# Kernel optimization log

Hardware: AMD Instinct MI355X
Metric: run time of the kernel (lower is better)

## Reference

```python
import jax, jax.numpy as jnp
import numpy as np

B, N, NC = 16, 102000, 35        # batch, raw YOLOv7@1280 predictions, num classes
IMG = 1280                        # input image size
CONF_THRESH = 0.25
IOU_THRESH = 0.45
PRE_TOPK = 1024                   # candidates kept before IoU suppression (yolov7 max_nms analogue)
MAX_DET = 300                     # padded detections per image (yolov7 max_det)


def setup_inputs() -> dict:
    key = jax.random.key(0)
    kxy, kwh, kobj, kcls = jax.random.split(key, 4)
    xy = jax.random.uniform(kxy, (B, N, 2), dtype=jnp.float32) * IMG        # box centers in pixels
    wh = jax.random.uniform(kwh, (B, N, 2), dtype=jnp.float32) * 96.0 + 4.0  # box sizes
    obj = jax.random.uniform(kobj, (B, N, 1), dtype=jnp.float32)            # objectness
    cls = jax.random.uniform(kcls, (B, N, NC), dtype=jnp.float32)           # class scores
    pred = jnp.concatenate([xy, wh, obj, cls], axis=-1)  # [B, N, 5+NC]
    return {"pred": pred}


def _xywh2xyxy(xywh):
    xy, wh = xywh[..., :2], xywh[..., 2:4]
    return jnp.concatenate([xy - wh * 0.5, xy + wh * 0.5], axis=-1)


def _iou_matrix(b):
    # b: [K, 4] xyxy -> [K, K] pairwise IoU
    area = jnp.clip(b[:, 2] - b[:, 0], 0.0) * jnp.clip(b[:, 3] - b[:, 1], 0.0)
    lt = jnp.maximum(b[:, None, :2], b[None, :, :2])
    rb = jnp.minimum(b[:, None, 2:], b[None, :, 2:])
    wh = jnp.clip(rb - lt, 0.0)
    inter = wh[..., 0] * wh[..., 1]
    return inter / (area[:, None] + area[None, :] - inter + 1e-7)


def _nms_single(boxes, scores, cls_id):
    # boxes: [N,4] xyxy, scores: [N] (0 where below conf thresh), cls_id: [N] float
    s, idx = jax.lax.top_k(scores, PRE_TOPK)
    b = boxes[idx]
    c = cls_id[idx]
    iou = _iou_matrix(b)              # [K, K]
    valid = s > 0.0
    ar = jnp.arange(PRE_TOPK)

    def body(suppressed, i):
        keep_i = valid[i] & ~suppressed[i]
        suppressed = suppressed | (keep_i & (iou[i] > IOU_THRESH) & (ar > i))
        return suppressed, keep_i

    _, keep = jax.lax.scan(body, jnp.zeros(PRE_TOPK, bool), ar)
    final = jnp.where(keep, s, 0.0)
    fs, fidx = jax.lax.top_k(final, MAX_DET)
    # [MAX_DET, 6] = x1, y1, x2, y2, conf, cls (conf==0 rows are padding)
    return jnp.concatenate([b[fidx], fs[:, None], c[fidx][:, None]], axis=-1)


def reference(pred):
    # yolov7 non_max_suppression, class-agnostic, best-class per box
    boxes = _xywh2xyxy(pred[..., :4])                    # [B, N, 4]
    obj = pred[..., 4]                                   # [B, N]
    cls_scores = pred[..., 5:] * obj[..., None]          # obj_conf * cls_conf
    conf = jnp.max(cls_scores, axis=-1)                  # [B, N]
    cls_id = jnp.argmax(cls_scores, axis=-1).astype(pred.dtype)
    cand = (obj > CONF_THRESH) & (conf > CONF_THRESH)    # candidate filter
    scores = jnp.where(cand, conf, 0.0)
    return jax.vmap(_nms_single)(boxes, scores, cls_id)  # [B, MAX_DET, 6]
```

## Files before the change

kernel.cpp:

```cpp
#include <hip/hip_runtime.h>
#include <stdint.h>

#define BB 16
#define NN 102000
#define NCLS 35
#define RSTRIDE 40
#define PRE 1024
#define CAP 2048
#define MAXDET 300
#define NBUCK 4096
#define CONF_T 0.25f
#define IOU_T 0.45f
#define BUCK_BASE 0x3E800000u
#define SROWS 256

#define SCORES_OFF ((size_t)0)
#define SCORES_BYTES ((size_t)BB * NN * 4)
#define GHIST_OFF (SCORES_OFF + SCORES_BYTES)
#define GHIST_BYTES ((size_t)BB * NBUCK * 4)
#define CUT_OFF (GHIST_OFF + GHIST_BYTES)
#define BOXES_OFF (CUT_OFF + 64)
#define BOXES_BYTES ((size_t)BB * PRE * 16)
#define SVAL_OFF (BOXES_OFF + BOXES_BYTES)
#define SVAL_BYTES ((size_t)BB * PRE * 4)
#define CLS_OFF (SVAL_OFF + SVAL_BYTES)
#define CLS_BYTES ((size_t)BB * PRE * 4)
#define MASK_OFF (CLS_OFF + CLS_BYTES)
#define MASK_BYTES ((size_t)BB * PRE * 16 * 8)

__global__ __launch_bounds__(256) void k_score(const float* __restrict__ pred,
                                               float* __restrict__ scores,
                                               unsigned int* __restrict__ ghist) {
    __shared__ float4 lds4[SROWS * 9];
    int b = blockIdx.y, tid = threadIdx.x;
    int rowBase = blockIdx.x * SROWS;
    int nrows = NN - rowBase; if (nrows > SROWS) nrows = SROWS;
    const float4* gp = (const float4*)(pred + ((size_t)b * NN + rowBase) * RSTRIDE);
    int nf4 = nrows * 9;
    for (int it = tid; it < nf4; it += 256) {
        int r = it / 9;
        int c = it - r * 9;
        lds4[r * 9 + c] = gp[r * 10 + 1 + c];
    }
    __syncthreads();
    if (tid < nrows) {
        const float4* row4 = &lds4[tid * 9];
        float4 v0 = row4[0];
        float obj = v0.x;
        float score = 0.0f;
        if (obj > CONF_T) {
            float best = v0.y * obj;
            best = fmaxf(best, v0.z * obj);
            best = fmaxf(best, v0.w * obj);
#pragma unroll
            for (int c = 1; c < 9; ++c) {
                float4 v = row4[c];
                best = fmaxf(best, v.x * obj);
                best = fmaxf(best, v.y * obj);
                best = fmaxf(best, v.z * obj);
                best = fmaxf(best, v.w * obj);
            }
            if (best > CONF_T) score = best;
        }
        scores[(size_t)b * NN + rowBase + tid] = score;
        if (score > 0.0f) {
            unsigned int bits = __float_as_uint(score);
            unsigned int bk = (bits - BUCK_BASE) >> 12;
            if (bk > NBUCK - 1u) bk = NBUCK - 1u;
            atomicAdd(&ghist[b * NBUCK + bk], 1u);
        }
    }
}

__global__ __launch_bounds__(1024) void k_cut(const unsigned int* __restrict__ ghist,
                                              unsigned int* __restrict__ cutv) {
    __shared__ int sA[1024], sB[1024];
    __shared__ int cutB;
    int b = blockIdx.x, tid = threadIdx.x;
    if (tid == 0) cutB = 0;
    __syncthreads();
    const unsigned int* gh = ghist + b * NBUCK;
    int h0 = gh[4 * tid + 0], h1 = gh[4 * tid + 1];
    int h2 = gh[4 * tid + 2], h3 = gh[4 * tid + 3];
    sA[tid] = h0 + h1 + h2 + h3;
    __syncthreads();
    int* src = sA;
    int* dst = sB;
    for (int off = 1; off < 1024; off <<= 1) {
        int x = src[tid];
        if (tid + off < 1024) x += src[tid + off];
        dst[tid] = x;
        __syncthreads();
        int* t_ = src; src = dst; dst = t_;
    }
    int nxt = (tid + 1 < 1024) ? src[tid + 1] : 0;
    int s3 = h3 + nxt;
    int s2 = h2 + s3;
    int s1 = h1 + s2;
    int s0 = h0 + s1;
    if (s0 >= PRE && s1 < PRE) cutB = 4 * tid + 0;
    if (s1 >= PRE && s2 < PRE) cutB = 4 * tid + 1;
    if (s2 >= PRE && s3 < PRE) cutB = 4 * tid + 2;
    if (s3 >= PRE && nxt < PRE) cutB = 4 * tid + 3;
    __syncthreads();
    if (tid == 0) cutv[b] = (unsigned int)cutB;
}

__global__ __launch_bounds__(1024) void k_sort(const float* __restrict__ scores,
                                               const unsigned int* __restrict__ cutv,
                                               const float* __restrict__ pred,
                                               float4* __restrict__ boxesWS,
                                               float* __restrict__ svalWS,
                                               float* __restrict__ clsWS) {
    __shared__ unsigned long long keys[CAP];
    __shared__ unsigned int nloc;
    int b = blockIdx.x, tid = threadIdx.x;
    unsigned int cut = cutv[b];
    if (tid == 0) nloc = 0u;
    for (int k = tid; k < CAP; k += 1024) keys[k] = 0ull;
    __syncthreads();
    const float4* sb4 = (const float4*)(scores + (size_t)b * NN);
    for (int it = tid; it < NN / 4; it += 1024) {
        float4 s4 = sb4[it];
        float sv[4] = {s4.x, s4.y, s4.z, s4.w};
#pragma unroll
        for (int u = 0; u < 4; ++u) {
            float s = sv[u];
            if (s > 0.0f) {
                unsigned int bits = __float_as_uint(s);
                unsigned int bk = (bits - BUCK_BASE) >> 12;
                if (bk > NBUCK - 1u) bk = NBUCK - 1u;
                if (bk >= cut) {
                    unsigned int pos = atomicAdd(&nloc, 1u);
                    unsigned int idx = (unsigned int)(it * 4 + u);
                    if (pos < CAP)
                        keys[pos] = ((unsigned long long)bits << 32) |
                                    (unsigned int)(~idx);
                }
            }
        }
    }
    __syncthreads();
    for (int k = 2; k <= CAP; k <<= 1) {
        for (int j = k >> 1; j > 0; j >>= 1) {
            int p = ((tid & ~(j - 1)) << 1) | (tid & (j - 1));
            int q = p | j;
            unsigned long long a = keys[p], c = keys[q];
            bool desc = (p & k) == 0;
            bool sw = desc ? (a < c) : (a > c);
            if (sw) { keys[p] = c; keys[q] = a; }
            __syncthreads();
        }
    }
    unsigned long long key = keys[tid];
    unsigned int bits = (unsigned int)(key >> 32);
    unsigned int idx = ~(unsigned int)key;
    float sc = __uint_as_float(bits);
    if (bits == 0u || idx >= NN) { idx = 0; sc = 0.0f; }
    const float4* row = (const float4*)(pred + ((size_t)b * NN + idx) * RSTRIDE);
    float4 r0 = row[0];
    float4 r1 = row[1];
    float obj = r1.x;
    float best = r1.y * obj; int bj = 0;
    float p1 = r1.z * obj; if (p1 > best) { best = p1; bj = 1; }
    float p2 = r1.w * obj; if (p2 > best) { best = p2; bj = 2; }
#pragma unroll
    for (int kk = 2; kk <= 9; ++kk) {
        float4 r = row[kk];
        int base = (kk - 2) * 4 + 3;
        float q0 = r.x * obj; if (q0 > best) { best = q0; bj = base + 0; }
        float q1 = r.y * obj; if (q1 > best) { best = q1; bj = base + 1; }
        float q2 = r.z * obj; if (q2 > best) { best = q2; bj = base + 2; }
        float q3 = r.w * obj; if (q3 > best) { best = q3; bj = base + 3; }
    }
    float hx = r0.z * 0.5f;
    float hy = r0.w * 0.5f;
    boxesWS[b * PRE + tid] = make_float4(r0.x - hx, r0.y - hy, r0.x + hx, r0.y + hy);
    svalWS[b * PRE + tid] = sc;
    clsWS[b * PRE + tid] = (float)bj;
}

__global__ __launch_bounds__(256) void k_mask(const float4* __restrict__ boxesWS,
                                              const float* __restrict__ svalWS,
                                              unsigned long long* __restrict__ maskC) {
    __shared__ float bx1[PRE], by1[PRE], bx2[PRE], by2[PRE], bar[PRE], bsv[PRE];
    int b = blockIdx.y, tid = threadIdx.x;
    for (int i = tid; i < PRE; i += 256) {
        float4 bx = boxesWS[b * PRE + i];
        bx1[i] = bx.x; by1[i] = bx.y; bx2[i] = bx.z; by2[i] = bx.w;
        float aw = fmaxf(bx.z - bx.x, 0.0f);
        float ah = fmaxf(bx.w - bx.y, 0.0f);
        bar[i] = aw * ah;
        bsv[i] = svalWS[b * PRE + i];
    }
    __syncthreads();
    int j = blockIdx.x * 4 + (tid >> 6);
    int lane = tid & 63;
    float jx1 = bx1[j], jy1 = by1[j], jx2 = bx2[j], jy2 = by2[j], ja = bar[j];
    unsigned long long* out = maskC + ((size_t)b * PRE + j) * 16;
    for (int c = 0; c < 16; ++c) {
        unsigned long long word = 0ull;
        if (c * 64 < j) {
            int i = c * 64 + lane;
            bool bit = false;
            if (i < j && bsv[i] > 0.0f) {
                float ltx = fmaxf(bx1[i], jx1), lty = fmaxf(by1[i], jy1);
                float rbx = fminf(bx2[i], jx2), rby = fminf(by2[i], jy2);
                float wx = fmaxf(rbx - ltx, 0.0f);
                float wy = fmaxf(rby - lty, 0.0f);
                float inter = wx * wy;
                float denom = ((bar[i] + ja) - inter) + 1e-7f;
                bit = (inter / denom) > IOU_T;
            }
            word = __ballot(bit);
        }
        if (lane == 0) out[c] = word;
    }
}

__global__ __launch_bounds__(1024) void k_nms_out(const float4* __restrict__ boxesWS,
                                                  const float* __restrict__ svalWS,
                                                  const float* __restrict__ clsWS,
                                                  const unsigned long long* __restrict__ maskC,
                                                  float* __restrict__ out) {
    __shared__ unsigned long long supp[16], nsupp[16];
    __shared__ int changed;
    __shared__ int wtot[16], woff[17];
    int b = blockIdx.x, tid = threadIdx.x;
    int lane = tid & 63, w = tid >> 6;
    unsigned long long cm[16];
    const unsigned long long* mrow = maskC + ((size_t)b * PRE + tid) * 16;
#pragma unroll
    for (int k = 0; k < 16; ++k) cm[k] = mrow[k];
    float sv = svalWS[b * PRE + tid];
    if (tid < 16) supp[tid] = 0ull;
    __syncthreads();
    for (int it = 0; it < PRE + 2; ++it) {
        bool nb = false;
#pragma unroll
        for (int k = 0; k < 16; ++k) nb |= ((cm[k] & ~supp[k]) != 0ull);
        unsigned long long word = __ballot(nb);
        __syncthreads();
        if (lane == 0) nsupp[w] = word;
        if (tid == 0) changed = 0;
        __syncthreads();
        if (tid < 16) {
            if (nsupp[tid] != supp[tid]) changed = 1;
            supp[tid] = nsupp[tid];
        }
        __syncthreads();
        if (!changed) break;
    }
    bool keep = (sv > 0.0f) && !((supp[w] >> lane) & 1ull);
    unsigned long long km = __ballot(keep);
    int lp = __popcll(km & ((lane == 0) ? 0ull : ((1ull << lane) - 1ull)));
    if (lane == 0) wtot[w] = __popcll(km);
    __syncthreads();
    if (tid == 0) {
        int acc = 0;
        for (int k = 0; k < 16; ++k) { woff[k] = acc; acc += wtot[k]; }
        woff[16] = acc;
    }
    __syncthreads();
    int K = woff[16];
    int keptExcl = woff[w] + lp;
    int slot = keep ? keptExcl : (K + (tid - keptExcl));
    if (slot < MAXDET) {
        float4 bx = boxesWS[b * PRE + tid];
        float cv = clsWS[b * PRE + tid];
        float* o = out + ((size_t)b * MAXDET + slot) * 6;
        o[0] = bx.x; o[1] = bx.y; o[2] = bx.z; o[3] = bx.w;
        o[4] = keep ? sv : 0.0f;
        o[5] = cv;
    }
}

extern "C" void kernel_launch(void* const* d_in, const int* in_sizes, int n_in,
                              void* d_out, int out_size, void* d_ws, size_t ws_size,
                              hipStream_t stream) {
    const float* pred = (const float*)d_in[0];
    float* out = (float*)d_out;
    char* ws = (char*)d_ws;
    float* scores = (float*)(ws + SCORES_OFF);
    unsigned int* ghist = (unsigned int*)(ws + GHIST_OFF);
    unsigned int* cutv = (unsigned int*)(ws + CUT_OFF);
    float4* boxesWS = (float4*)(ws + BOXES_OFF);
    float* svalWS = (float*)(ws + SVAL_OFF);
    float* clsWS = (float*)(ws + CLS_OFF);
    unsigned long long* maskC = (unsigned long long*)(ws + MASK_OFF);

    hipMemsetAsync(ws + GHIST_OFF, 0, GHIST_BYTES, stream);
    k_score<<<dim3((NN + SROWS - 1) / SROWS, BB), 256, 0, stream>>>(pred, scores, ghist);
    k_cut<<<BB, 1024, 0, stream>>>(ghist, cutv);
    k_sort<<<BB, 1024, 0, stream>>>(scores, cutv, pred, boxesWS, svalWS, clsWS);
    k_mask<<<dim3(PRE / 4, BB), 256, 0, stream>>>(boxesWS, svalWS, maskC);
    k_nms_out<<<BB, 1024, 0, stream>>>(boxesWS, svalWS, clsWS, maskC, out);
}
```

Measured before the change: 434.7 us.

## Use per-wave tiles in score kernel and fuse cut with sort kernel

The score kernel now gives each 64-lane wave its own 64-row tile. The wave copies full 40-float rows contiguously into LDS with no block-wide barrier, in place of the strided 9-of-10 float4 gather. The separate histogram-cut kernel is merged into the sort kernel, so the cut bucket stays in shared memory, which removes one launch and the global cut round-trip. The trade-off is that the score kernel now also loads the unused first float4 of each row, and the fused kernel uses more shared memory.

```diff
diff --git a/kernel.cpp b/kernel.cpp
--- a/kernel.cpp
+++ b/kernel.cpp
@@ -12,14 +12,13 @@
 #define CONF_T 0.25f
 #define IOU_T 0.45f
 #define BUCK_BASE 0x3E800000u
-#define SROWS 256
+#define TROWS 64
 
 #define SCORES_OFF ((size_t)0)
 #define SCORES_BYTES ((size_t)BB * NN * 4)
 #define GHIST_OFF (SCORES_OFF + SCORES_BYTES)
 #define GHIST_BYTES ((size_t)BB * NBUCK * 4)
-#define CUT_OFF (GHIST_OFF + GHIST_BYTES)
-#define BOXES_OFF (CUT_OFF + 64)
+#define BOXES_OFF (GHIST_OFF + GHIST_BYTES)
 #define BOXES_BYTES ((size_t)BB * PRE * 16)
 #define SVAL_OFF (BOXES_OFF + BOXES_BYTES)
 #define SVAL_BYTES ((size_t)BB * PRE * 4)
@@ -31,21 +30,24 @@
 __global__ __launch_bounds__(256) void k_score(const float* __restrict__ pred,
                                                float* __restrict__ scores,
                                                unsigned int* __restrict__ ghist) {
-    __shared__ float4 lds4[SROWS * 9];
-    int b = blockIdx.y, tid = threadIdx.x;
-    int rowBase = blockIdx.x * SROWS;
-    int nrows = NN - rowBase; if (nrows > SROWS) nrows = SROWS;
+    __shared__ float4 lds4[4 * TROWS * 10];
+    int b = blockIdx.y;
+    int wv = threadIdx.x >> 6, lane = threadIdx.x & 63;
+    int tile = blockIdx.x * 4 + wv;
+    int rowBase = tile * TROWS;
+    if (rowBase >= NN) return;
+    int nrows = NN - rowBase; if (nrows > TROWS) nrows = TROWS;
+    int nf4 = nrows * 10;
     const float4* gp = (const float4*)(pred + ((size_t)b * NN + rowBase) * RSTRIDE);
-    int nf4 = nrows * 9;
-    for (int it = tid; it < nf4; it += 256) {
-        int r = it / 9;
-        int c = it - r * 9;
-        lds4[r * 9 + c] = gp[r * 10 + 1 + c];
-    }
-    __syncthreads();
-    if (tid < nrows) {
-        const float4* row4 = &lds4[tid * 9];
-        float4 v0 = row4[0];
+    float4* wlds = &lds4[wv * TROWS * 10];
+#pragma unroll
+    for (int k = 0; k < 10; ++k) {
+        int idx = k * 64 + lane;
+        if (idx < nf4) wlds[idx] = gp[idx];
+    }
+    if (lane < nrows) {
+        const float4* row4 = &wlds[lane * 10];
+        float4 v0 = row4[1];
         float obj = v0.x;
         float score = 0.0f;
         if (obj > CONF_T) {
@@ -53,7 +55,7 @@
             best = fmaxf(best, v0.z * obj);
             best = fmaxf(best, v0.w * obj);
 #pragma unroll
-            for (int c = 1; c < 9; ++c) {
+            for (int c = 2; c < 10; ++c) {
                 float4 v = row4[c];
                 best = fmaxf(best, v.x * obj);
                 best = fmaxf(best, v.y * obj);
@@ -62,7 +64,7 @@
             }
             if (best > CONF_T) score = best;
         }
-        scores[(size_t)b * NN + rowBase + tid] = score;
+        scores[(size_t)b * NN + rowBase + lane] = score;
         if (score > 0.0f) {
             unsigned int bits = __float_as_uint(score);
             unsigned int bk = (bits - BUCK_BASE) >> 12;
@@ -72,12 +74,19 @@
     }
 }
 
-__global__ __launch_bounds__(1024) void k_cut(const unsigned int* __restrict__ ghist,
-                                              unsigned int* __restrict__ cutv) {
+__global__ __launch_bounds__(1024) void k_cutsort(const unsigned int* __restrict__ ghist,
+                                                  const float* __restrict__ scores,
+                                                  const float* __restrict__ pred,
+                                                  float4* __restrict__ boxesWS,
+                                                  float* __restrict__ svalWS,
+                                                  float* __restrict__ clsWS) {
+    __shared__ unsigned long long keys[CAP];
     __shared__ int sA[1024], sB[1024];
     __shared__ int cutB;
+    __shared__ unsigned int nloc;
     int b = blockIdx.x, tid = threadIdx.x;
-    if (tid == 0) cutB = 0;
+    if (tid == 0) { cutB = 0; nloc = 0u; }
+    keys[tid] = 0ull; keys[tid + 1024] = 0ull;
     __syncthreads();
     const unsigned int* gh = ghist + b * NBUCK;
     int h0 = gh[4 * tid + 0], h1 = gh[4 * tid + 1];
@@ -103,22 +112,7 @@
     if (s2 >= PRE && s3 < PRE) cutB = 4 * tid + 2;
     if (s3 >= PRE && nxt < PRE) cutB = 4 * tid + 3;
     __syncthreads();
-    if (tid == 0) cutv[b] = (unsigned int)cutB;
-}
-
-__global__ __launch_bounds__(1024) void k_sort(const float* __restrict__ scores,
-                                               const unsigned int* __restrict__ cutv,
-                                               const float* __restrict__ pred,
-                                               float4* __restrict__ boxesWS,
-                                               float* __restrict__ svalWS,
-                                               float* __restrict__ clsWS) {
-    __shared__ unsigned long long keys[CAP];
-    __shared__ unsigned int nloc;
-    int b = blockIdx.x, tid = threadIdx.x;
-    unsigned int cut = cutv[b];
-    if (tid == 0) nloc = 0u;
-    for (int k = tid; k < CAP; k += 1024) keys[k] = 0ull;
-    __syncthreads();
+    unsigned int cut = (unsigned int)cutB;
     const float4* sb4 = (const float4*)(scores + (size_t)b * NN);
     for (int it = tid; it < NN / 4; it += 1024) {
         float4 s4 = sb4[it];
@@ -283,16 +277,16 @@
     char* ws = (char*)d_ws;
     float* scores = (float*)(ws + SCORES_OFF);
     unsigned int* ghist = (unsigned int*)(ws + GHIST_OFF);
-    unsigned int* cutv = (unsigned int*)(ws + CUT_OFF);
     float4* boxesWS = (float4*)(ws + BOXES_OFF);
     float* svalWS = (float*)(ws + SVAL_OFF);
     float* clsWS = (float*)(ws + CLS_OFF);
     unsigned long long* maskC = (unsigned long long*)(ws + MASK_OFF);
 
+    int tilesPerBatch = (NN + TROWS - 1) / TROWS;
+    int blocksX = (tilesPerBatch + 3) / 4;
     hipMemsetAsync(ws + GHIST_OFF, 0, GHIST_BYTES, stream);
-    k_score<<<dim3((NN + SROWS - 1) / SROWS, BB), 256, 0, stream>>>(pred, scores, ghist);
-    k_cut<<<BB, 1024, 0, stream>>>(ghist, cutv);
-    k_sort<<<BB, 1024, 0, stream>>>(scores, cutv, pred, boxesWS, svalWS, clsWS);
+    k_score<<<dim3(blocksX, BB), 256, 0, stream>>>(pred, scores, ghist);
+    k_cutsort<<<BB, 1024, 0, stream>>>(ghist, scores, pred, boxesWS, svalWS, clsWS);
     k_mask<<<dim3(PRE / 4, BB), 256, 0, stream>>>(boxesWS, svalWS, maskC);
     k_nms_out<<<BB, 1024, 0, stream>>>(boxesWS, svalWS, clsWS, maskC, out);
 }
```

Measured after the change: 435.2 us. About the same (+0.1%).
